# Performance work log

Hardware: AMD Instinct MI355X
Metric: run time of the kernel (lower is better)

## Reference

```python
import jax, jax.numpy as jnp
import numpy as np

B, S, E, H = 4, 2048, 1024, 16
HD = E // H  # 64 head dim


def setup_inputs() -> dict:
    key = jax.random.key(0)
    ks = jax.random.split(key, 6)
    x = jax.random.normal(ks[0], (B, S, E), dtype=jnp.float32)
    mask = jax.random.randint(ks[1], (B, S, S), 0, 2, dtype=jnp.int32)
    # per-head qkv Linear(E -> 3*HD), stacked over heads: weight [H, 3*HD, E]
    lim = 1.0 / np.sqrt(E)
    Wqkv = jax.random.uniform(ks[2], (H, 3 * HD, E), minval=-lim, maxval=lim, dtype=jnp.float32)
    bqkv = jax.random.uniform(ks[3], (H, 3 * HD), minval=-lim, maxval=lim, dtype=jnp.float32)
    Wo = jax.random.uniform(ks[4], (E, E), minval=-lim, maxval=lim, dtype=jnp.float32)
    bo = jax.random.uniform(ks[5], (E,), minval=-lim, maxval=lim, dtype=jnp.float32)
    return {"x": x, "mask": mask, "Wqkv": Wqkv, "bqkv": bqkv, "Wo": Wo, "bo": bo}


def reference(x, mask, Wqkv, bqkv, Wo, bo):
    # fused per-head qkv projection: [B,S,E] x [H,3HD,E] -> [B,H,S,3HD]
    qkv = jnp.einsum('bse,hfe->bhsf', x, Wqkv) + bqkv[None, :, None, :]
    q, k, v = jnp.split(qkv, 3, axis=-1)  # each [B,H,S,HD]
    scale = 1.0 / jnp.sqrt(jnp.float32(HD))
    scores = jnp.einsum('bhqd,bhkd->bhqk', q, k) * scale  # [B,H,S,S]
    # NOTE: original masked_fill sets masked scores to 0.0 (not -inf)
    scores = jnp.where(mask[:, None, :, :] == 1, 0.0, scores)
    attn = jax.nn.softmax(scores, axis=-1)
    ctx = jnp.einsum('bhqk,bhkd->bhqd', attn, v)  # [B,H,S,HD]
    ctx = ctx.transpose(0, 2, 1, 3).reshape(B, S, E)  # concat heads
    return ctx @ Wo.T + bo
```

## Files before the change

### kernel.cpp

```cpp
#include <hip/hip_runtime.h>
#include <stdint.h>

#define B_ 4
#define S_ 2048
#define E_ 1024
#define H_ 16
#define HD_ 64

typedef __attribute__((ext_vector_type(8))) short bf16x8;
typedef __attribute__((ext_vector_type(4))) float f32x4;

__device__ __forceinline__ ushort f2b(float f) {
    union { float f; uint32_t u; } c; c.f = f;
    return (ushort)((c.u + 0x8000u) >> 16);
}

__device__ __forceinline__ uint32_t pkbf(float a, float b) {
    union { float f; uint32_t u; } ca, cb; ca.f = a; cb.f = b;
#if __has_builtin(__builtin_amdgcn_perm)
    return __builtin_amdgcn_perm(cb.u + 0x8000u, ca.u + 0x8000u, 0x07060302u);
#else
    return (uint32_t)f2b(a) | ((uint32_t)f2b(b) << 16);
#endif
}

#if __has_builtin(__builtin_amdgcn_exp2f)
#define EXP2(x) __builtin_amdgcn_exp2f(x)
#else
#define EXP2(x) exp2f(x)
#endif

__device__ __forceinline__ void gl2lds16(const ushort* g, const ushort* l) {
    __builtin_amdgcn_global_load_lds(
        (const __attribute__((address_space(1))) unsigned int*)g,
        (__attribute__((address_space(3))) unsigned int*)l,
        16, 0, 0);
}
__device__ __forceinline__ void gl2lds16raw(const void* g, const void* l) {
    __builtin_amdgcn_global_load_lds(
        (const __attribute__((address_space(1))) unsigned int*)g,
        (__attribute__((address_space(3))) unsigned int*)l,
        16, 0, 0);
}

__global__ __launch_bounds__(256) void cvt_all(
    const float* __restrict__ x, const float* __restrict__ wq, const float* __restrict__ wo,
    ushort* __restrict__ xb, ushort* __restrict__ wqb, ushort* __restrict__ wob) {
    int i = blockIdx.x * 256 + threadIdx.x;
    const float* src; ushort* dst; int off;
    if (i < 2097152)      { src = x;  dst = xb;  off = i; }
    else if (i < 2883584) { src = wq; dst = wqb; off = i - 2097152; }
    else                  { src = wo; dst = wob; off = i - 2883584; }
    float4 f = ((const float4*)src)[off];
    ushort4 o;
    o.x = f2b(f.x); o.y = f2b(f.y); o.z = f2b(f.z); o.w = f2b(f.w);
    ((ushort4*)dst)[off] = o;
}

__global__ __launch_bounds__(256) void pack_mask(const int* __restrict__ mask,
                                                 uint32_t* __restrict__ mb) {
    int i = blockIdx.x * 256 + threadIdx.x;
    unsigned long long bal = __ballot(mask[i] == 1);
    int lane = threadIdx.x & 63;
    if (lane < 2) {
        int b = i >> 22, q = (i >> 11) & 2047, c = i & 2047;
        int kt = c >> 6;
        mb[((uint64_t)(b * 32 + kt) * 2048 + q) * 2 + lane] =
            (lane == 0) ? (uint32_t)bal : (uint32_t)(bal >> 32);
    }
}

template <int KD>
__device__ __forceinline__ void gemm_bt_core(
    const ushort* __restrict__ A, const ushort* __restrict__ Bm,
    int m0, int n0, ushort* As, ushort* Bs, f32x4 (&acc)[4][4])
{
    const int tid  = threadIdx.x;
    const int lane = tid & 63;
    const int wave = tid >> 6;
    const int wm = wave >> 1, wn = wave & 1;
    const int fr = lane & 15;
    const int fk = (lane >> 4) * 8;
    const int lrow = lane >> 2;
    const int lk   = (lane & 3) * 8;

    const f32x4 fz = {0.f, 0.f, 0.f, 0.f};
#pragma unroll
    for (int i = 0; i < 4; ++i)
#pragma unroll
        for (int j = 0; j < 4; ++j) acc[i][j] = fz;

    for (int kt = 0; kt < KD / 32; ++kt) {
        const int k0 = kt * 32;
        __syncthreads();
#pragma unroll
        for (int t = 0; t < 2; ++t) {
            const int r0 = t * 64 + wave * 16;
            gl2lds16(&A [(uint64_t)(m0 + r0 + lrow) * KD + k0 + lk], &As[r0 * 32]);
            gl2lds16(&Bm[(uint64_t)(n0 + r0 + lrow) * KD + k0 + lk], &Bs[r0 * 32]);
        }
        __syncthreads();
        bf16x8 af[4], bfr[4];
#pragma unroll
        for (int i = 0; i < 4; ++i)
            af[i] = *(const bf16x8*)&As[(wm * 64 + i * 16 + fr) * 32 + fk];
#pragma unroll
        for (int j = 0; j < 4; ++j)
            bfr[j] = *(const bf16x8*)&Bs[(wn * 64 + j * 16 + fr) * 32 + fk];
#pragma unroll
        for (int i = 0; i < 4; ++i)
#pragma unroll
            for (int j = 0; j < 4; ++j)
                acc[i][j] = __builtin_amdgcn_mfma_f32_16x16x32_bf16(af[i], bfr[j], acc[i][j], 0, 0, 0);
    }
}

__global__ __launch_bounds__(256) void qkv_gemm(
    const ushort* __restrict__ xb, const ushort* __restrict__ wb,
    const float* __restrict__ bqkv,
    ushort* __restrict__ qo, ushort* __restrict__ ko, ushort* __restrict__ vto)
{
    __shared__ ushort As[128 * 32];
    __shared__ ushort Bs[128 * 32];
    f32x4 acc[4][4];
    const int m0 = blockIdx.x * 128;
    const int n0 = blockIdx.y * 128;
    gemm_bt_core<1024>(xb, wb, m0, n0, As, Bs, acc);

    const int lane = threadIdx.x & 63, wave = threadIdx.x >> 6;
    const int wm = wave >> 1, wn = wave & 1;
    const int col = lane & 15, rg = lane >> 4;
    const float QSC = 0.125f * 1.4426950408889634f;
#pragma unroll
    for (int j = 0; j < 4; ++j) {
        const int n = n0 + wn * 64 + j * 16 + col;
        const int h = n / 192, f = n % 192;
        const float bias = bqkv[n];
#pragma unroll
        for (int i2 = 0; i2 < 4; ++i2) {
            const int mbase = m0 + wm * 64 + i2 * 16 + rg * 4;
            if (f < 128) {
#pragma unroll
                for (int v = 0; v < 4; ++v) {
                    const int m = mbase + v;
                    const int b = m >> 11, s = m & 2047;
                    const float val = acc[i2][j][v] + bias;
                    if (f < 64) qo[((uint64_t)(b * 16 + h) * 2048 + s) * 64 + f]        = f2b(val * QSC);
                    else        ko[((uint64_t)(b * 16 + h) * 2048 + s) * 64 + (f - 64)] = f2b(val);
                }
            } else {
                const int b = mbase >> 11, s = mbase & 2047;
                ushort4 pk;
                pk.x = f2b(acc[i2][j][0] + bias);
                pk.y = f2b(acc[i2][j][1] + bias);
                pk.z = f2b(acc[i2][j][2] + bias);
                pk.w = f2b(acc[i2][j][3] + bias);
                *(ushort4*)&vto[((uint64_t)(b * 16 + h) * 64 + (f - 128)) * 2048 + s] = pk;
            }
        }
    }
}

__global__ __launch_bounds__(256, 3) void attn_kernel(
    const ushort* __restrict__ qa, const ushort* __restrict__ ka,
    const ushort* __restrict__ vta, const uint32_t* __restrict__ mbits,
    ushort* __restrict__ ctxo)
{
    __shared__ __align__(16) ushort SMEM[128 * 64];
    __shared__ __align__(16) ushort Ks[2][64 * 64];
    __shared__ __align__(16) ushort Vts[2][64 * 64];
    __shared__ __align__(16) uint32_t Ms[2][256];

    const int bid = blockIdx.x;
    const int qb = bid & 15;
    const int bh = bid >> 4;
    const int b = bh >> 4;
    const int tid = threadIdx.x, lane = tid & 63, wave = tid >> 6;
    const int col = lane & 15, rg = lane >> 4;

    const uint64_t bhoff = (uint64_t)bh * (S_ * 64);
    const ushort* qp = qa + bhoff + (uint64_t)qb * 128 * 64;
    const ushort* kp = ka + bhoff;
    const ushort* vp = vta + bhoff;
    const uint32_t* mkb = mbits + ((uint64_t)(b * 32) * 2048 + qb * 128) * 2;

    const int lr = lane >> 3;
    const int usw = (lane & 7) ^ lr;
    const int r0s = wave * 16 + lr;
    const int r1s = r0s + 8;
    const int sg0 = (r0s & 32) | ((r0s & 12) << 1) | ((r0s & 16) >> 2) | (r0s & 3);
    const int sg1 = (r1s & 32) | ((r1s & 12) << 1) | ((r1s & 16) >> 2) | (r1s & 3);
    const int kb0 = sg0 * 64 + usw * 8;
    const int kb1 = sg1 * 64 + usw * 8;
    const int vb0 = r0s * 2048 + usw * 8;
    const int vb1 = r1s * 2048 + usw * 8;
    const int ldst0 = wave * 1024;
    const int ldst1 = ldst0 + 512;

#pragma unroll
    for (int t4 = 0; t4 < 4; ++t4) {
        const int o = (wave * 4 + t4) * 512;
        gl2lds16(&qp[o + lane * 8], &SMEM[o]);
    }
    gl2lds16(&kp[kb0], &Ks[0][ldst0]);
    gl2lds16(&kp[kb1], &Ks[0][ldst1]);
    gl2lds16(&vp[vb0], &Vts[0][ldst0]);
    gl2lds16(&vp[vb1], &Vts[0][ldst1]);
    if (wave == 0) gl2lds16raw(mkb + lane * 4, &Ms[0][0]);
    __syncthreads();

    bf16x8 aq[2][2];
#pragma unroll
    for (int i = 0; i < 2; ++i)
#pragma unroll
        for (int k2 = 0; k2 < 2; ++k2)
            aq[i][k2] = *(const bf16x8*)&SMEM[(wave * 32 + i * 16 + col) * 64 + k2 * 32 + rg * 8];

    const f32x4 fz = {0.f, 0.f, 0.f, 0.f};
    f32x4 acc[4][2];
#pragma unroll
    for (int dt = 0; dt < 4; ++dt)
#pragma unroll
        for (int i = 0; i < 2; ++i) acc[dt][i] = fz;
    f32x4 acc5[2] = {fz, fz};

    bf16x8 vone;
#pragma unroll
    for (int e = 0; e < 8; ++e) vone[e] = (short)0x3F80;

    uint32_t bsel[2][4];
#pragma unroll
    for (int p = 0; p < 2; ++p)
#pragma unroll
        for (int v = 0; v < 4; ++v) bsel[p][v] = 1u << (rg * 8 + p * 4 + v);

    const int u0 = (rg ^ (col & 7)) << 3;

    for (int kt = 0; kt < 32; ++kt) {
        const int buf = kt & 1;
        if (kt < 31) {
            const int knext = (kt + 1) * 4096;
            gl2lds16(&kp[knext + kb0], &Ks[buf ^ 1][ldst0]);
            gl2lds16(&kp[knext + kb1], &Ks[buf ^ 1][ldst1]);
            gl2lds16(&vp[vb0 + (kt + 1) * 64], &Vts[buf ^ 1][ldst0]);
            gl2lds16(&vp[vb1 + (kt + 1) * 64], &Vts[buf ^ 1][ldst1]);
            if (wave == 0) gl2lds16raw(mkb + (uint64_t)(kt + 1) * 4096 + lane * 4,
                                       &Ms[buf ^ 1][0]);
        }

        f32x4 sc[2][4];
#pragma unroll
        for (int j = 0; j < 4; ++j) {
            bf16x8 bk0 = *(const bf16x8*)&Ks[buf][(j * 16 + col) * 64 + u0];
            bf16x8 bk1 = *(const bf16x8*)&Ks[buf][(j * 16 + col) * 64 + (u0 ^ 32)];
#pragma unroll
            for (int i = 0; i < 2; ++i) {
                f32x4 z = __builtin_amdgcn_mfma_f32_16x16x32_bf16(bk0, aq[i][0], fz, 0, 0, 0);
                sc[i][j] = __builtin_amdgcn_mfma_f32_16x16x32_bf16(bk1, aq[i][1], z, 0, 0, 0);
            }
        }

        bf16x8 bp[2][2];
#pragma unroll
        for (int i = 0; i < 2; ++i) {
            const uint2 mw = *(const uint2*)&Ms[buf][(wave * 32 + i * 16 + col) * 2];
            union { uint32_t w[4]; bf16x8 v; } p0, p1;
#pragma unroll
            for (int j = 0; j < 4; ++j) {
                const uint32_t w = (j & 2) ? mw.y : mw.x;
                const int p = j & 1;
                float pe[4];
#pragma unroll
                for (int v = 0; v < 4; ++v) {
                    const float s = (w & bsel[p][v]) ? 0.f : sc[i][j][v];
                    pe[v] = EXP2(s);
                }
                const uint32_t lo = pkbf(pe[0], pe[1]);
                const uint32_t hi = pkbf(pe[2], pe[3]);
                if (j < 2) { p0.w[p * 2] = lo; p0.w[p * 2 + 1] = hi; }
                else       { p1.w[p * 2] = lo; p1.w[p * 2 + 1] = hi; }
            }
            bp[i][0] = p0.v;
            bp[i][1] = p1.v;
        }

#pragma unroll
        for (int i = 0; i < 2; ++i) {
            acc5[i] = __builtin_amdgcn_mfma_f32_16x16x32_bf16(vone, bp[i][0], acc5[i], 0, 0, 0);
            acc5[i] = __builtin_amdgcn_mfma_f32_16x16x32_bf16(vone, bp[i][1], acc5[i], 0, 0, 0);
        }
#pragma unroll
        for (int dt = 0; dt < 4; ++dt) {
            bf16x8 av0 = *(const bf16x8*)&Vts[buf][(dt * 16 + col) * 64 + u0];
            bf16x8 av1 = *(const bf16x8*)&Vts[buf][(dt * 16 + col) * 64 + (u0 ^ 32)];
#pragma unroll
            for (int i = 0; i < 2; ++i) {
                acc[dt][i] = __builtin_amdgcn_mfma_f32_16x16x32_bf16(av0, bp[i][0], acc[dt][i], 0, 0, 0);
                acc[dt][i] = __builtin_amdgcn_mfma_f32_16x16x32_bf16(av1, bp[i][1], acc[dt][i], 0, 0, 0);
            }
        }
        __syncthreads();
    }

    float linv[2];
#pragma unroll
    for (int i = 0; i < 2; ++i) linv[i] = 1.0f / acc5[i][0];

#pragma unroll
    for (int dt = 0; dt < 4; ++dt)
#pragma unroll
        for (int i = 0; i < 2; ++i) {
            const int q = wave * 32 + i * 16 + col;
            const int d = dt * 16 + rg * 4;
            const int gg = (d >> 3) ^ (q & 7);
            ushort4 pk;
            pk.x = f2b(acc[dt][i][0] * linv[i]);
            pk.y = f2b(acc[dt][i][1] * linv[i]);
            pk.z = f2b(acc[dt][i][2] * linv[i]);
            pk.w = f2b(acc[dt][i][3] * linv[i]);
            *(ushort4*)&SMEM[q * 64 + gg * 8 + (d & 7)] = pk;
        }
    __syncthreads();
    const int h = bh & 15;
    const uint64_t obase = (uint64_t)(b * S_ + qb * 128) * E_ + (uint64_t)h * 64;
#pragma unroll
    for (int t4 = 0; t4 < 4; ++t4) {
        const int id = tid + t4 * 256;
        const int r = id >> 3, c8 = id & 7;
        *(bf16x8*)&ctxo[obase + (uint64_t)r * E_ + c8 * 8] =
            *(const bf16x8*)&SMEM[r * 64 + ((c8 ^ (r & 7)) << 3)];
    }
}

__global__ __launch_bounds__(256) void out_gemm(
    const ushort* __restrict__ ctxb, const ushort* __restrict__ wob,
    const float* __restrict__ bo, float* __restrict__ out)
{
    __shared__ ushort As[128 * 32];
    __shared__ ushort Bs[128 * 32];
    f32x4 acc[4][4];
    const int m0 = blockIdx.x * 128;
    const int n0 = blockIdx.y * 128;
    gemm_bt_core<1024>(ctxb, wob, m0, n0, As, Bs, acc);

    const int lane = threadIdx.x & 63, wave = threadIdx.x >> 6;
    const int wm = wave >> 1, wn = wave & 1;
    const int col = lane & 15, rg = lane >> 4;
#pragma unroll
    for (int j = 0; j < 4; ++j) {
        const int n = n0 + wn * 64 + j * 16 + col;
        const float bias = bo[n];
#pragma unroll
        for (int i2 = 0; i2 < 4; ++i2) {
            const int mb2 = m0 + wm * 64 + i2 * 16 + rg * 4;
#pragma unroll
            for (int v = 0; v < 4; ++v)
                out[(uint64_t)(mb2 + v) * 1024 + n] = acc[i2][j][v] + bias;
        }
    }
}

extern "C" void kernel_launch(void* const* d_in, const int* in_sizes, int n_in,
                              void* d_out, int out_size, void* d_ws, size_t ws_size,
                              hipStream_t stream)
{
    const float* x    = (const float*)d_in[0];
    const int*   mask = (const int*)d_in[1];
    const float* Wqkv = (const float*)d_in[2];
    const float* bqkv = (const float*)d_in[3];
    const float* Wo   = (const float*)d_in[4];
    const float* bo   = (const float*)d_in[5];
    float* out = (float*)d_out;

    char* p = (char*)d_ws;
    ushort* xb  = (ushort*)p; p += (size_t)8388608 * 2;
    ushort* wqb = (ushort*)p; p += (size_t)3145728 * 2;
    ushort* wob = (ushort*)p; p += (size_t)1048576 * 2;
    ushort* qo  = (ushort*)p; p += (size_t)8388608 * 2;
    ushort* ko  = (ushort*)p; p += (size_t)8388608 * 2;
    ushort* vto = (ushort*)p; p += (size_t)8388608 * 2;
    ushort* ctx = (ushort*)p; p += (size_t)8388608 * 2;
    uint32_t* mb = (uint32_t*)p;

    cvt_all<<<12288, 256, 0, stream>>>(x, Wqkv, Wo, xb, wqb, wob);
    pack_mask<<<65536, 256, 0, stream>>>(mask, mb);
    qkv_gemm<<<dim3(64, 24), 256, 0, stream>>>(xb, wqb, bqkv, qo, ko, vto);
    attn_kernel<<<1024, 256, 0, stream>>>(qo, ko, vto, mb, ctx);
    out_gemm<<<dim3(64, 8), 256, 0, stream>>>(ctx, wob, bo, out);
}
```

Before: 370.7 us.

## Shrink attention LDS footprint, load Q and mask via registers, raise occupancy

The attention kernel drops the separate Q staging buffer and mask LDS buffers. Q fragments are now loaded straight from global memory into registers, and mask words are prefetched into registers one tile ahead. The context output buffer aliases the second K/V buffer, cutting LDS use to 32KB so launch bounds can target 4 blocks per CU. It also remaps block IDs so blocks sharing a head are spread out, adds s_setprio around the MFMA sections, and unrolls the loop by two. The aim is higher occupancy and less LDS traffic, at the risk of register pressure under the tighter bound and uncoalesced direct Q loads.

```diff
diff --git a/kernel.cpp b/kernel.cpp
--- a/kernel.cpp
+++ b/kernel.cpp
@@ -31,12 +31,6 @@
 #endif
 
 __device__ __forceinline__ void gl2lds16(const ushort* g, const ushort* l) {
-    __builtin_amdgcn_global_load_lds(
-        (const __attribute__((address_space(1))) unsigned int*)g,
-        (__attribute__((address_space(3))) unsigned int*)l,
-        16, 0, 0);
-}
-__device__ __forceinline__ void gl2lds16raw(const void* g, const void* l) {
     __builtin_amdgcn_global_load_lds(
         (const __attribute__((address_space(1))) unsigned int*)g,
         (__attribute__((address_space(3))) unsigned int*)l,
@@ -161,19 +155,21 @@
     }
 }
 
-__global__ __launch_bounds__(256, 3) void attn_kernel(
+__global__ __launch_bounds__(256, 4) void attn_kernel(
     const ushort* __restrict__ qa, const ushort* __restrict__ ka,
     const ushort* __restrict__ vta, const uint32_t* __restrict__ mbits,
     ushort* __restrict__ ctxo)
 {
-    __shared__ __align__(16) ushort SMEM[128 * 64];
-    __shared__ __align__(16) ushort Ks[2][64 * 64];
-    __shared__ __align__(16) ushort Vts[2][64 * 64];
-    __shared__ __align__(16) uint32_t Ms[2][256];
+    __shared__ __align__(16) ushort LDSH[16384];
+    ushort* const Ks0 = LDSH;
+    ushort* const Vt0 = LDSH + 4096;
+    ushort* const Ks1 = LDSH + 8192;
+    ushort* const Vt1 = LDSH + 12288;
+    ushort* const CTX = LDSH + 8192;
 
     const int bid = blockIdx.x;
-    const int qb = bid & 15;
-    const int bh = bid >> 4;
+    const int bh = (bid & 7) * 8 + (bid >> 7);
+    const int qb = (bid >> 3) & 15;
     const int b = bh >> 4;
     const int tid = threadIdx.x, lane = tid & 63, wave = tid >> 6;
     const int col = lane & 15, rg = lane >> 4;
@@ -182,7 +178,8 @@
     const ushort* qp = qa + bhoff + (uint64_t)qb * 128 * 64;
     const ushort* kp = ka + bhoff;
     const ushort* vp = vta + bhoff;
-    const uint32_t* mkb = mbits + ((uint64_t)(b * 32) * 2048 + qb * 128) * 2;
+    const uint32_t* mk0 = mbits + ((uint64_t)(b * 32) * 2048 + qb * 128 + wave * 32 + col) * 2;
+    const uint32_t* mk1 = mk0 + 32;
 
     const int lr = lane >> 3;
     const int usw = (lane & 7) ^ lr;
@@ -197,24 +194,21 @@
     const int ldst0 = wave * 1024;
     const int ldst1 = ldst0 + 512;
 
-#pragma unroll
-    for (int t4 = 0; t4 < 4; ++t4) {
-        const int o = (wave * 4 + t4) * 512;
-        gl2lds16(&qp[o + lane * 8], &SMEM[o]);
-    }
-    gl2lds16(&kp[kb0], &Ks[0][ldst0]);
-    gl2lds16(&kp[kb1], &Ks[0][ldst1]);
-    gl2lds16(&vp[vb0], &Vts[0][ldst0]);
-    gl2lds16(&vp[vb1], &Vts[0][ldst1]);
-    if (wave == 0) gl2lds16raw(mkb + lane * 4, &Ms[0][0]);
+    bf16x8 aq[2][2];
+#pragma unroll
+    for (int i = 0; i < 2; ++i)
+#pragma unroll
+        for (int k2 = 0; k2 < 2; ++k2)
+            aq[i][k2] = *(const bf16x8*)&qp[(wave * 32 + i * 16 + col) * 64 + k2 * 32 + rg * 8];
+
+    gl2lds16(&kp[kb0], &Ks0[ldst0]);
+    gl2lds16(&kp[kb1], &Ks0[ldst1]);
+    gl2lds16(&vp[vb0], &Vt0[ldst0]);
+    gl2lds16(&vp[vb1], &Vt0[ldst1]);
+    uint2 mc0 = *(const uint2*)mk0;
+    uint2 mc1 = *(const uint2*)mk1;
+    uint2 mn0 = mc0, mn1 = mc1;
     __syncthreads();
-
-    bf16x8 aq[2][2];
-#pragma unroll
-    for (int i = 0; i < 2; ++i)
-#pragma unroll
-        for (int k2 = 0; k2 < 2; ++k2)
-            aq[i][k2] = *(const bf16x8*)&SMEM[(wave * 32 + i * 16 + col) * 64 + k2 * 32 + rg * 8];
 
     const f32x4 fz = {0.f, 0.f, 0.f, 0.f};
     f32x4 acc[4][2];
@@ -236,34 +230,42 @@
 
     const int u0 = (rg ^ (col & 7)) << 3;
 
+#pragma unroll 2
     for (int kt = 0; kt < 32; ++kt) {
         const int buf = kt & 1;
+        const ushort* const Ksb = buf ? Ks1 : Ks0;
+        const ushort* const Vtb = buf ? Vt1 : Vt0;
+        ushort* const Ksn = buf ? Ks0 : Ks1;
+        ushort* const Vtn = buf ? Vt0 : Vt1;
+
         if (kt < 31) {
             const int knext = (kt + 1) * 4096;
-            gl2lds16(&kp[knext + kb0], &Ks[buf ^ 1][ldst0]);
-            gl2lds16(&kp[knext + kb1], &Ks[buf ^ 1][ldst1]);
-            gl2lds16(&vp[vb0 + (kt + 1) * 64], &Vts[buf ^ 1][ldst0]);
-            gl2lds16(&vp[vb1 + (kt + 1) * 64], &Vts[buf ^ 1][ldst1]);
-            if (wave == 0) gl2lds16raw(mkb + (uint64_t)(kt + 1) * 4096 + lane * 4,
-                                       &Ms[buf ^ 1][0]);
+            gl2lds16(&kp[knext + kb0], &Ksn[ldst0]);
+            gl2lds16(&kp[knext + kb1], &Ksn[ldst1]);
+            gl2lds16(&vp[vb0 + (kt + 1) * 64], &Vtn[ldst0]);
+            gl2lds16(&vp[vb1 + (kt + 1) * 64], &Vtn[ldst1]);
+            mn0 = *(const uint2*)(mk0 + (uint64_t)(kt + 1) * 4096);
+            mn1 = *(const uint2*)(mk1 + (uint64_t)(kt + 1) * 4096);
         }
 
         f32x4 sc[2][4];
+        __builtin_amdgcn_s_setprio(1);
 #pragma unroll
         for (int j = 0; j < 4; ++j) {
-            bf16x8 bk0 = *(const bf16x8*)&Ks[buf][(j * 16 + col) * 64 + u0];
-            bf16x8 bk1 = *(const bf16x8*)&Ks[buf][(j * 16 + col) * 64 + (u0 ^ 32)];
+            bf16x8 bk0 = *(const bf16x8*)&Ksb[(j * 16 + col) * 64 + u0];
+            bf16x8 bk1 = *(const bf16x8*)&Ksb[(j * 16 + col) * 64 + (u0 ^ 32)];
 #pragma unroll
             for (int i = 0; i < 2; ++i) {
                 f32x4 z = __builtin_amdgcn_mfma_f32_16x16x32_bf16(bk0, aq[i][0], fz, 0, 0, 0);
                 sc[i][j] = __builtin_amdgcn_mfma_f32_16x16x32_bf16(bk1, aq[i][1], z, 0, 0, 0);
             }
         }
+        __builtin_amdgcn_s_setprio(0);
 
         bf16x8 bp[2][2];
 #pragma unroll
         for (int i = 0; i < 2; ++i) {
-            const uint2 mw = *(const uint2*)&Ms[buf][(wave * 32 + i * 16 + col) * 2];
+            const uint2 mw = i ? mc1 : mc0;
             union { uint32_t w[4]; bf16x8 v; } p0, p1;
 #pragma unroll
             for (int j = 0; j < 4; ++j) {
@@ -284,6 +286,7 @@
             bp[i][1] = p1.v;
         }
 
+        __builtin_amdgcn_s_setprio(1);
 #pragma unroll
         for (int i = 0; i < 2; ++i) {
             acc5[i] = __builtin_amdgcn_mfma_f32_16x16x32_bf16(vone, bp[i][0], acc5[i], 0, 0, 0);
@@ -291,15 +294,17 @@
         }
 #pragma unroll
         for (int dt = 0; dt < 4; ++dt) {
-            bf16x8 av0 = *(const bf16x8*)&Vts[buf][(dt * 16 + col) * 64 + u0];
-            bf16x8 av1 = *(const bf16x8*)&Vts[buf][(dt * 16 + col) * 64 + (u0 ^ 32)];
+            bf16x8 av0 = *(const bf16x8*)&Vtb[(dt * 16 + col) * 64 + u0];
+            bf16x8 av1 = *(const bf16x8*)&Vtb[(dt * 16 + col) * 64 + (u0 ^ 32)];
 #pragma unroll
             for (int i = 0; i < 2; ++i) {
                 acc[dt][i] = __builtin_amdgcn_mfma_f32_16x16x32_bf16(av0, bp[i][0], acc[dt][i], 0, 0, 0);
                 acc[dt][i] = __builtin_amdgcn_mfma_f32_16x16x32_bf16(av1, bp[i][1], acc[dt][i], 0, 0, 0);
             }
         }
+        __builtin_amdgcn_s_setprio(0);
         __syncthreads();
+        mc0 = mn0; mc1 = mn1;
     }
 
     float linv[2];
@@ -318,7 +323,7 @@
             pk.y = f2b(acc[dt][i][1] * linv[i]);
             pk.z = f2b(acc[dt][i][2] * linv[i]);
             pk.w = f2b(acc[dt][i][3] * linv[i]);
-            *(ushort4*)&SMEM[q * 64 + gg * 8 + (d & 7)] = pk;
+            *(ushort4*)&CTX[q * 64 + gg * 8 + (d & 7)] = pk;
         }
     __syncthreads();
     const int h = bh & 15;
@@ -328,7 +333,7 @@
         const int id = tid + t4 * 256;
         const int r = id >> 3, c8 = id & 7;
         *(bf16x8*)&ctxo[obase + (uint64_t)r * E_ + c8 * 8] =
-            *(const bf16x8*)&SMEM[r * 64 + ((c8 ^ (r & 7)) << 3)];
+            *(const bf16x8*)&CTX[r * 64 + ((c8 ^ (r & 7)) << 3)];
     }
 }
 
```

Measured after the change: 374.6 us. Within noise of the previous version (+1.1%).
